# Kernel tuning notes

Measured on AMD Instinct MI355X. Metric: run time of the kernel, lower is better.

## Reference

```python
import jax, jax.numpy as jnp
import numpy as np

D_MODEL = 1024
NUM_HEADS = 16
D_K = D_MODEL // NUM_HEADS


def setup_inputs() -> dict:
    key = jax.random.key(0)
    ks = jax.random.split(key, 12)
    B, S = 2, 2048
    s = 1.0 / np.sqrt(D_MODEL)
    inp = {
        "query": jax.random.normal(ks[0], (B, S, D_MODEL), jnp.float32),
        "key": jax.random.normal(ks[1], (B, S, D_MODEL), jnp.float32),
        "value": jax.random.normal(ks[2], (B, S, D_MODEL), jnp.float32),
        "Wq": jax.random.normal(ks[3], (D_MODEL, D_MODEL), jnp.float32) * s,
        "bq": jax.random.normal(ks[4], (D_MODEL,), jnp.float32) * s,
        "Wk": jax.random.normal(ks[5], (D_MODEL, D_MODEL), jnp.float32) * s,
        "bk": jax.random.normal(ks[6], (D_MODEL,), jnp.float32) * s,
        "Wv": jax.random.normal(ks[7], (D_MODEL, D_MODEL), jnp.float32) * s,
        "bv": jax.random.normal(ks[8], (D_MODEL,), jnp.float32) * s,
        "Wo": jax.random.normal(ks[9], (D_MODEL, D_MODEL), jnp.float32) * s,
        "bo": jax.random.normal(ks[10], (D_MODEL,), jnp.float32) * s,
    }
    return inp


def _split_heads(x):
    B, S, _ = x.shape
    return x.reshape(B, S, NUM_HEADS, D_K).transpose(0, 2, 1, 3)  # [B,H,S,Dk]


def reference(query, key, value, Wq, bq, Wk, bk, Wv, bv, Wo, bo):
    # Linear projections (torch Linear: x @ W.T + b)
    Q = _split_heads(query @ Wq.T + bq)
    K = _split_heads(key @ Wk.T + bk)
    V = _split_heads(value @ Wv.T + bv)
    scale = 1.0 / jnp.sqrt(jnp.asarray(D_K, Q.dtype))
    scores = jnp.einsum('bhqd,bhkd->bhqk', Q, K) * scale  # [B,H,S,S]
    attn = jax.nn.softmax(scores, axis=-1)
    # dropout is identity in eval mode
    x = jnp.einsum('bhqk,bhkd->bhqd', attn, V)
    B, H, S, Dk = x.shape
    x = x.transpose(0, 2, 1, 3).reshape(B, S, H * Dk)
    return x @ Wo.T + bo
```

## Files before the change

kernel.cpp:

```cpp
#include <hip/hip_runtime.h>
#include <hip/hip_bf16.h>

typedef __bf16 bf16;
typedef __attribute__((ext_vector_type(4))) __bf16 bf16x4;
typedef __attribute__((ext_vector_type(8))) __bf16 bf16x8;
typedef __attribute__((ext_vector_type(4))) float f32x4;
typedef __attribute__((ext_vector_type(16))) float f32x16;
typedef unsigned int u32;

#define D_MODEL 1024
#define NHEADS 16
#define DK 64
#define BATCH 2
#define SEQ 2048
#define NTOK (BATCH * SEQ)

#define QSCALE 0.18033688011112042f
#define DEFER_THR 8.0f

__device__ __forceinline__ u32 cvtpk_bf16(float lo, float hi) {
  u32 r;
  asm("v_cvt_pk_bf16_f32 %0, %1, %2" : "=v"(r) : "v"(lo), "v"(hi));
  return r;
}
__device__ __forceinline__ void plswap(u32& a, u32& b) {
  asm("v_permlane32_swap_b32 %0, %1" : "+v"(a), "+v"(b));
}
__device__ __forceinline__ float fast_exp2(float x) {
#if __has_builtin(__builtin_amdgcn_exp2f)
  return __builtin_amdgcn_exp2f(x);
#else
  return exp2f(x);
#endif
}
__device__ __forceinline__ float xhalf_max(float x) {
  return fmaxf(x, __shfl_xor(x, 32));
}
__device__ __forceinline__ float xhalf_add(float x) {
  return x + __shfl_xor(x, 32);
}

__device__ __forceinline__ int frag_off_q(int s, int d) {
  return ((s >> 5) << 11) + ((d >> 4) << 9) + ((((d >> 3) & 1) * 32 + (s & 31)) << 3) + (d & 7);
}
__device__ __forceinline__ int frag_off_k(int s, int d) {
  return ((s >> 6) << 12) + ((((s >> 5) & 1) * 4 + (d >> 4)) << 9) +
         ((((d >> 3) & 1) * 32 + (s & 31)) << 3) + (d & 7);
}
__device__ __forceinline__ int frag_off_v(int s, int d) {
  return ((s >> 6) << 12) + (((d >> 5) * 4 + ((s >> 4) & 3)) << 9) +
         ((((s >> 3) & 1) * 32 + (d & 31)) << 3) + (s & 7);
}

__global__ __launch_bounds__(256) void cvt3_kernel(
    const float* __restrict__ s0, const float* __restrict__ s1, const float* __restrict__ s2,
    bf16* __restrict__ d0, bf16* __restrict__ d1, bf16* __restrict__ d2, int n4) {
  int i = blockIdx.x * blockDim.x + threadIdx.x;
  if (i >= n4) return;
  const float* s = blockIdx.y == 0 ? s0 : blockIdx.y == 1 ? s1 : s2;
  bf16* d = blockIdx.y == 0 ? d0 : blockIdx.y == 1 ? d1 : d2;
  float4 v = reinterpret_cast<const float4*>(s)[i];
  bf16x4 o;
  o[0] = (bf16)v.x; o[1] = (bf16)v.y; o[2] = (bf16)v.z; o[3] = (bf16)v.w;
  reinterpret_cast<bf16x4*>(d)[i] = o;
}

__global__ __launch_bounds__(256) void cvt4_kernel(
    const float* __restrict__ s0, const float* __restrict__ s1,
    const float* __restrict__ s2, const float* __restrict__ s3,
    bf16* __restrict__ d0, bf16* __restrict__ d1, bf16* __restrict__ d2, bf16* __restrict__ d3,
    int n4) {
  int i = blockIdx.x * blockDim.x + threadIdx.x;
  if (i >= n4) return;
  const float* s = blockIdx.y == 0 ? s0 : blockIdx.y == 1 ? s1 : blockIdx.y == 2 ? s2 : s3;
  bf16* d = blockIdx.y == 0 ? d0 : blockIdx.y == 1 ? d1 : blockIdx.y == 2 ? d2 : d3;
  float4 v = reinterpret_cast<const float4*>(s)[i];
  bf16x4 o;
  o[0] = (bf16)v.x; o[1] = (bf16)v.y; o[2] = (bf16)v.z; o[3] = (bf16)v.w;
  reinterpret_cast<bf16x4*>(d)[i] = o;
}

#define ASYNC_COPY16(gptr, lptr)                                                \
  __builtin_amdgcn_global_load_lds(                                             \
      (__attribute__((address_space(1))) void*)(gptr),                          \
      (__attribute__((address_space(3))) void*)(lptr), 16, 0, 0)

struct ProjArgs {
  const bf16* A[3];
  const bf16* W[3];
  const float* bias[3];
  bf16* out[3];
};

__global__ __launch_bounds__(256) void gemm_proj(ProjArgs pa, int K) {
  __shared__ bf16 As[128][32];
  __shared__ bf16 Bs[128][32];
  const int z = blockIdx.z;
  const bf16* A = pa.A[z];
  const bf16* Bw = pa.W[z];
  const int m0 = blockIdx.x * 128;
  const int n0 = blockIdx.y * 128;

  const int t = threadIdx.x;
  const int wave = t >> 6;
  const int lane = t & 63;
  const int wr = (wave >> 1) * 64;
  const int wc = (wave & 1) * 64;
  const int r4 = lane >> 2;
  const int c8 = (lane & 3) * 8;
  const int fr = lane & 15;
  const int fk = (lane >> 4) * 8;

  f32x4 acc[4][4] = {};

  for (int k0 = 0; k0 < K; k0 += 32) {
    ASYNC_COPY16(&A[(size_t)(m0 + wave * 16 + r4) * K + k0 + c8], &As[wave * 16][0]);
    ASYNC_COPY16(&A[(size_t)(m0 + 64 + wave * 16 + r4) * K + k0 + c8], &As[64 + wave * 16][0]);
    ASYNC_COPY16(&Bw[(size_t)(n0 + wave * 16 + r4) * K + k0 + c8], &Bs[wave * 16][0]);
    ASYNC_COPY16(&Bw[(size_t)(n0 + 64 + wave * 16 + r4) * K + k0 + c8], &Bs[64 + wave * 16][0]);
    __syncthreads();

    bf16x8 af[4], bfr[4];
#pragma unroll
    for (int m = 0; m < 4; m++)
      af[m] = *reinterpret_cast<const bf16x8*>(&As[wr + m * 16 + fr][fk]);
#pragma unroll
    for (int n = 0; n < 4; n++)
      bfr[n] = *reinterpret_cast<const bf16x8*>(&Bs[wc + n * 16 + fr][fk]);
#pragma unroll
    for (int m = 0; m < 4; m++)
#pragma unroll
      for (int n = 0; n < 4; n++)
        acc[m][n] = __builtin_amdgcn_mfma_f32_16x16x32_bf16(af[m], bfr[n], acc[m][n], 0, 0, 0);
    __syncthreads();
  }

  const float scale = (z == 0) ? QSCALE : 1.0f;
  const float* bias = pa.bias[z];
  bf16* out = pa.out[z];
#pragma unroll
  for (int m = 0; m < 4; m++) {
#pragma unroll
    for (int n = 0; n < 4; n++) {
      const int col = n0 + wc + n * 16 + fr;
      const float bv = bias[col];
#pragma unroll
      for (int j = 0; j < 4; j++) {
        const int row = m0 + wr + m * 16 + (lane >> 4) * 4 + j;
        const float v = (acc[m][n][j] + bv) * scale;
        const int b = row >> 11;
        const int s = row & (SEQ - 1);
        const int h = col >> 6;
        const int d = col & (DK - 1);
        const size_t base = (size_t)(b * NHEADS + h) * SEQ * DK;
        int off;
        if (z == 0)      off = frag_off_q(s, d);
        else if (z == 1) off = frag_off_k(s, d);
        else             off = frag_off_v(s, d);
        out[base + off] = (bf16)v;
      }
    }
  }
}

#define TM 128
#define TN 64
#define BK 32

__global__ __launch_bounds__(256) void gemm_out(
    const bf16* __restrict__ A, const bf16* __restrict__ Bw,
    const float* __restrict__ bias, float* __restrict__ out, int K) {
  __shared__ bf16 As[TM][BK];
  __shared__ bf16 Bs[TN][BK];
  const int m0 = blockIdx.x * TM;
  const int n0 = blockIdx.y * TN;

  const int t = threadIdx.x;
  const int wave = t >> 6;
  const int lane = t & 63;
  const int wr = (wave >> 1) * 64;
  const int wc = (wave & 1) * 32;
  const int r4 = lane >> 2;
  const int c8 = (lane & 3) * 8;
  const int fr = lane & 15;
  const int fk = (lane >> 4) * 8;

  f32x4 acc[4][2] = {};
  for (int k0 = 0; k0 < K; k0 += BK) {
    ASYNC_COPY16(&A[(size_t)(m0 + wave * 16 + r4) * K + k0 + c8], &As[wave * 16][0]);
    ASYNC_COPY16(&A[(size_t)(m0 + 64 + wave * 16 + r4) * K + k0 + c8], &As[64 + wave * 16][0]);
    ASYNC_COPY16(&Bw[(size_t)(n0 + wave * 16 + r4) * K + k0 + c8], &Bs[wave * 16][0]);
    __syncthreads();

    bf16x8 af[4], bfr[2];
#pragma unroll
    for (int m = 0; m < 4; m++)
      af[m] = *reinterpret_cast<const bf16x8*>(&As[wr + m * 16 + fr][fk]);
#pragma unroll
    for (int n = 0; n < 2; n++)
      bfr[n] = *reinterpret_cast<const bf16x8*>(&Bs[wc + n * 16 + fr][fk]);
#pragma unroll
    for (int m = 0; m < 4; m++)
#pragma unroll
      for (int n = 0; n < 2; n++)
        acc[m][n] = __builtin_amdgcn_mfma_f32_16x16x32_bf16(af[m], bfr[n], acc[m][n], 0, 0, 0);
    __syncthreads();
  }

#pragma unroll
  for (int m = 0; m < 4; m++) {
#pragma unroll
    for (int n = 0; n < 2; n++) {
      const int col = n0 + wc + n * 16 + fr;
      const float bv = bias[col];
#pragma unroll
      for (int j = 0; j < 4; j++) {
        const int row = m0 + wr + m * 16 + (lane >> 4) * 4 + j;
        out[(size_t)row * D_MODEL + col] = acc[m][n][j] + bv;
      }
    }
  }
}

#define QBLK 32
#define KVBLK 64
#define NT (SEQ / KVBLK)

__global__ __launch_bounds__(256, 2) void attn_kernel(
    const bf16* __restrict__ Qf,
    const bf16* __restrict__ Kf,
    const bf16* __restrict__ Vf,
    bf16* __restrict__ X) {
  const int lane = threadIdx.x & 63;
  const int wave = threadIdx.x >> 6;

  const int i = blockIdx.x;
  const int xcd = i & 7;
  const int slot = i >> 3;
  const int hgrp = slot >> 4;
  const int xq = slot & 15;
  const int bh = xcd + 8 * hgrp;
  const int bb = bh >> 4, hh = bh & (NHEADS - 1);
  const int q0 = xq * (QBLK * 4) + wave * QBLK;
  const int row = lane & 31, hi = lane >> 5;

  const bf16* Qp = Qf + (size_t)bh * SEQ * DK + (size_t)q0 * DK;
  const bf16* Kp = Kf + (size_t)bh * SEQ * DK;
  const bf16* Vp = Vf + (size_t)bh * SEQ * DK;

  bf16x8 qf[4];
#pragma unroll
  for (int kd = 0; kd < 4; kd++)
    qf[kd] = *reinterpret_cast<const bf16x8*>(&Qp[kd * 512 + lane * 8]);

  f32x16 ot0, ot1;
#pragma unroll
  for (int r = 0; r < 16; r++) { ot0[r] = 0.f; ot1[r] = 0.f; }
  float m_run = -1e30f, l_run = 0.f;

  bf16x8 ka[2][4], kb2[2][4];

#define LOADK(dst, tt)                                                          \
  {                                                                             \
    const bf16* kbase_ = Kp + (size_t)(tt) * 4096 + lane * 8;                   \
    _Pragma("unroll") for (int hf = 0; hf < 2; hf++)                            \
        _Pragma("unroll") for (int kd = 0; kd < 4; kd++)                        \
            dst[hf][kd] = *reinterpret_cast<const bf16x8*>(                     \
                &kbase_[(hf * 4 + kd) * 512]);                                  \
  }

  LOADK(ka, 0)
  LOADK(kb2, 1)
  f32x16 sa0, sa1, sb0, sb1;
#pragma unroll
  for (int r = 0; r < 16; r++) { sa0[r] = 0.f; sa1[r] = 0.f; }
  __builtin_amdgcn_s_setprio(1);
#pragma unroll
  for (int kd = 0; kd < 4; kd++)
    sa0 = __builtin_amdgcn_mfma_f32_32x32x16_bf16(ka[0][kd], qf[kd], sa0, 0, 0, 0);
#pragma unroll
  for (int kd = 0; kd < 4; kd++)
    sa1 = __builtin_amdgcn_mfma_f32_32x32x16_bf16(ka[1][kd], qf[kd], sa1, 0, 0, 0);
  __builtin_amdgcn_s_setprio(0);

  auto pipe = [&](f32x16& SC0, f32x16& SC1, f32x16& SN0, f32x16& SN1,
                  bf16x8 (&KN)[2][4], bf16x8 (&KL)[2][4], int tc) {
#pragma unroll
    for (int r = 0; r < 16; r++) { SN0[r] = 0.f; SN1[r] = 0.f; }
    __builtin_amdgcn_s_setprio(1);
#pragma unroll
    for (int kd = 0; kd < 4; kd++)
      SN0 = __builtin_amdgcn_mfma_f32_32x32x16_bf16(KN[0][kd], qf[kd], SN0, 0, 0, 0);
#pragma unroll
    for (int kd = 0; kd < 4; kd++)
      SN1 = __builtin_amdgcn_mfma_f32_32x32x16_bf16(KN[1][kd], qf[kd], SN1, 0, 0, 0);
    __builtin_amdgcn_s_setprio(0);

    LOADK(KL, (tc + 2) & (NT - 1))

    bf16x8 vf[2][4];
    {
      const bf16* vbase_ = Vp + (size_t)tc * 4096 + lane * 8;
#pragma unroll
      for (int dh = 0; dh < 2; dh++)
#pragma unroll
        for (int ks = 0; ks < 4; ks++)
          vf[dh][ks] = *reinterpret_cast<const bf16x8*>(&vbase_[(dh * 4 + ks) * 512]);
    }

    float w16[16];
#pragma unroll
    for (int r = 0; r < 16; r++) w16[r] = fmaxf(SC0[r], SC1[r]);
#pragma unroll
    for (int r = 0; r < 8; r++) w16[r] = fmaxf(w16[r], w16[r + 8]);
#pragma unroll
    for (int r = 0; r < 4; r++) w16[r] = fmaxf(w16[r], w16[r + 4]);
    float mx = fmaxf(fmaxf(w16[0], w16[1]), fmaxf(w16[2], w16[3]));
    mx = xhalf_max(mx);
    if (__any(mx > m_run + DEFER_THR)) {
      const float mn = fmaxf(m_run, mx);
      const float alpha = fast_exp2(m_run - mn);
      m_run = mn;
      l_run *= alpha;
#pragma unroll
      for (int r = 0; r < 16; r++) { ot0[r] *= alpha; ot1[r] *= alpha; }
    }
    float p[32];
#pragma unroll
    for (int r = 0; r < 16; r++) p[r] = fast_exp2(SC0[r] - m_run);
#pragma unroll
    for (int r = 0; r < 16; r++) p[16 + r] = fast_exp2(SC1[r] - m_run);
    float a16[16];
#pragma unroll
    for (int r = 0; r < 16; r++) a16[r] = p[r] + p[r + 16];
#pragma unroll
    for (int r = 0; r < 8; r++) a16[r] += a16[r + 8];
#pragma unroll
    for (int r = 0; r < 4; r++) a16[r] += a16[r + 4];
    float rs = (a16[0] + a16[1]) + (a16[2] + a16[3]);
    l_run += xhalf_add(rs);

    u32 c[16];
#pragma unroll
    for (int i2 = 0; i2 < 8; i2++) c[i2] = cvtpk_bf16(p[2 * i2], p[2 * i2 + 1]);
#pragma unroll
    for (int i2 = 0; i2 < 8; i2++) c[8 + i2] = cvtpk_bf16(p[16 + 2 * i2], p[17 + 2 * i2]);
    plswap(c[0], c[2]);   plswap(c[1], c[3]);
    plswap(c[4], c[6]);   plswap(c[5], c[7]);
    plswap(c[8], c[10]);  plswap(c[9], c[11]);
    plswap(c[12], c[14]); plswap(c[13], c[15]);
    bf16x8 pbv[4];
#pragma unroll
    for (int ks = 0; ks < 4; ks++) {
      union { u32 u[4]; bf16x8 v; } pk;
      pk.u[0] = c[ks * 4 + 0]; pk.u[1] = c[ks * 4 + 1];
      pk.u[2] = c[ks * 4 + 2]; pk.u[3] = c[ks * 4 + 3];
      pbv[ks] = pk.v;
    }

    __builtin_amdgcn_s_setprio(1);
#pragma unroll
    for (int ks = 0; ks < 4; ks++) {
      ot0 = __builtin_amdgcn_mfma_f32_32x32x16_bf16(vf[0][ks], pbv[ks], ot0, 0, 0, 0);
      ot1 = __builtin_amdgcn_mfma_f32_32x32x16_bf16(vf[1][ks], pbv[ks], ot1, 0, 0, 0);
    }
    __builtin_amdgcn_s_setprio(0);
  };

  for (int t = 0; t < NT; t += 2) {
    pipe(sa0, sa1, sb0, sb1, kb2, ka, t);
    pipe(sb0, sb1, sa0, sa1, ka, kb2, t + 1);
  }

  const float inv = 1.0f / l_run;
  bf16* Xp = X + ((size_t)bb * SEQ + q0 + row) * D_MODEL + hh * DK;
#pragma unroll
  for (int g = 0; g < 4; g++) {
    bf16x4 w0, w1;
#pragma unroll
    for (int j = 0; j < 4; j++) {
      w0[j] = (bf16)(ot0[g * 4 + j] * inv);
      w1[j] = (bf16)(ot1[g * 4 + j] * inv);
    }
    *reinterpret_cast<bf16x4*>(&Xp[g * 8 + hi * 4]) = w0;
    *reinterpret_cast<bf16x4*>(&Xp[32 + g * 8 + hi * 4]) = w1;
  }
}

extern "C" void kernel_launch(void* const* d_in, const int* in_sizes, int n_in,
                              void* d_out, int out_size, void* d_ws, size_t ws_size,
                              hipStream_t stream) {
  const float* q  = (const float*)d_in[0];
  const float* k  = (const float*)d_in[1];
  const float* v  = (const float*)d_in[2];
  const float* Wq = (const float*)d_in[3];
  const float* bq = (const float*)d_in[4];
  const float* Wk = (const float*)d_in[5];
  const float* bk = (const float*)d_in[6];
  const float* Wv = (const float*)d_in[7];
  const float* bv = (const float*)d_in[8];
  const float* Wo = (const float*)d_in[9];
  const float* bo = (const float*)d_in[10];

  char* ws = (char*)d_ws;
  size_t off = 0;
  auto alloc = [&](size_t bytes) -> void* {
    void* p = ws + off;
    off += (bytes + 255) & ~(size_t)255;
    return p;
  };
  const size_t ACT = (size_t)NTOK * D_MODEL;
  const size_t WEL = (size_t)D_MODEL * D_MODEL;

  bf16* Xq  = (bf16*)alloc(ACT * 2);
  bf16* Xk  = (bf16*)alloc(ACT * 2);
  bf16* Xv  = (bf16*)alloc(ACT * 2);
  bf16* Wqb = (bf16*)alloc(WEL * 2);
  bf16* Wkb = (bf16*)alloc(WEL * 2);
  bf16* Wvb = (bf16*)alloc(WEL * 2);
  bf16* Wob = (bf16*)alloc(WEL * 2);
  bf16* Qfb = (bf16*)alloc(ACT * 2);
  bf16* Kfb = (bf16*)alloc(ACT * 2);
  bf16* Vfb = (bf16*)alloc(ACT * 2);
  bf16* Xa  = (bf16*)alloc(ACT * 2);

  {
    int n4 = (int)(ACT / 4);
    cvt3_kernel<<<dim3((n4 + 255) / 256, 3), dim3(256), 0, stream>>>(q, k, v, Xq, Xk, Xv, n4);
  }
  {
    int n4 = (int)(WEL / 4);
    cvt4_kernel<<<dim3((n4 + 255) / 256, 4), dim3(256), 0, stream>>>(
        Wq, Wk, Wv, Wo, Wqb, Wkb, Wvb, Wob, n4);
  }

  ProjArgs pa;
  pa.A[0] = Xq;  pa.A[1] = Xk;  pa.A[2] = Xv;
  pa.W[0] = Wqb; pa.W[1] = Wkb; pa.W[2] = Wvb;
  pa.bias[0] = bq; pa.bias[1] = bk; pa.bias[2] = bv;
  pa.out[0] = Qfb; pa.out[1] = Kfb; pa.out[2] = Vfb;
  gemm_proj<<<dim3(NTOK / 128, D_MODEL / 128, 3), dim3(256), 0, stream>>>(pa, D_MODEL);

  attn_kernel<<<dim3(512), dim3(256), 0, stream>>>(Qfb, Kfb, Vfb, Xa);

  gemm_out<<<dim3(NTOK / TM, D_MODEL / TN), dim3(256), 0, stream>>>(
      Xa, Wob, bo, (float*)d_out, D_MODEL);
}
```

Baseline: 136.9 us.

## Halve attention KV tile to 32 and widen output GEMM tile to 128x128

The attention kernel now processes 32 keys per pipeline step instead of 64. This halves the score registers and K prefetch buffers, which lowers register pressure, but doubles the number of loop iterations and the online-softmax max checks. The output projection GEMM moves from 128x64 to 128x128 tiles with a 4x4 MFMA accumulator per wave. That gives more reuse per LDS load, but launches half as many blocks.

```diff
diff --git a/kernel.cpp b/kernel.cpp
--- a/kernel.cpp
+++ b/kernel.cpp
@@ -163,46 +163,44 @@
   }
 }
 
-#define TM 128
-#define TN 64
-#define BK 32
-
 __global__ __launch_bounds__(256) void gemm_out(
     const bf16* __restrict__ A, const bf16* __restrict__ Bw,
     const float* __restrict__ bias, float* __restrict__ out, int K) {
-  __shared__ bf16 As[TM][BK];
-  __shared__ bf16 Bs[TN][BK];
-  const int m0 = blockIdx.x * TM;
-  const int n0 = blockIdx.y * TN;
+  __shared__ bf16 As[128][32];
+  __shared__ bf16 Bs[128][32];
+  const int m0 = blockIdx.x * 128;
+  const int n0 = blockIdx.y * 128;
 
   const int t = threadIdx.x;
   const int wave = t >> 6;
   const int lane = t & 63;
   const int wr = (wave >> 1) * 64;
-  const int wc = (wave & 1) * 32;
+  const int wc = (wave & 1) * 64;
   const int r4 = lane >> 2;
   const int c8 = (lane & 3) * 8;
   const int fr = lane & 15;
   const int fk = (lane >> 4) * 8;
 
-  f32x4 acc[4][2] = {};
-  for (int k0 = 0; k0 < K; k0 += BK) {
+  f32x4 acc[4][4] = {};
+
+  for (int k0 = 0; k0 < K; k0 += 32) {
     ASYNC_COPY16(&A[(size_t)(m0 + wave * 16 + r4) * K + k0 + c8], &As[wave * 16][0]);
     ASYNC_COPY16(&A[(size_t)(m0 + 64 + wave * 16 + r4) * K + k0 + c8], &As[64 + wave * 16][0]);
     ASYNC_COPY16(&Bw[(size_t)(n0 + wave * 16 + r4) * K + k0 + c8], &Bs[wave * 16][0]);
+    ASYNC_COPY16(&Bw[(size_t)(n0 + 64 + wave * 16 + r4) * K + k0 + c8], &Bs[64 + wave * 16][0]);
     __syncthreads();
 
-    bf16x8 af[4], bfr[2];
+    bf16x8 af[4], bfr[4];
 #pragma unroll
     for (int m = 0; m < 4; m++)
       af[m] = *reinterpret_cast<const bf16x8*>(&As[wr + m * 16 + fr][fk]);
 #pragma unroll
-    for (int n = 0; n < 2; n++)
+    for (int n = 0; n < 4; n++)
       bfr[n] = *reinterpret_cast<const bf16x8*>(&Bs[wc + n * 16 + fr][fk]);
 #pragma unroll
     for (int m = 0; m < 4; m++)
 #pragma unroll
-      for (int n = 0; n < 2; n++)
+      for (int n = 0; n < 4; n++)
         acc[m][n] = __builtin_amdgcn_mfma_f32_16x16x32_bf16(af[m], bfr[n], acc[m][n], 0, 0, 0);
     __syncthreads();
   }
@@ -210,7 +208,7 @@
 #pragma unroll
   for (int m = 0; m < 4; m++) {
 #pragma unroll
-    for (int n = 0; n < 2; n++) {
+    for (int n = 0; n < 4; n++) {
       const int col = n0 + wc + n * 16 + fr;
       const float bv = bias[col];
 #pragma unroll
@@ -223,7 +221,7 @@
 }
 
 #define QBLK 32
-#define KVBLK 64
+#define KVBLK 32
 #define NT (SEQ / KVBLK)
 
 __global__ __launch_bounds__(256, 2) void attn_kernel(
@@ -258,64 +256,55 @@
   for (int r = 0; r < 16; r++) { ot0[r] = 0.f; ot1[r] = 0.f; }
   float m_run = -1e30f, l_run = 0.f;
 
-  bf16x8 ka[2][4], kb2[2][4];
-
-#define LOADK(dst, tt)                                                          \
+  bf16x8 ka[4], kb[4];
+
+#define LOADK32(dst, tt)                                                        \
   {                                                                             \
-    const bf16* kbase_ = Kp + (size_t)(tt) * 4096 + lane * 8;                   \
-    _Pragma("unroll") for (int hf = 0; hf < 2; hf++)                            \
-        _Pragma("unroll") for (int kd = 0; kd < 4; kd++)                        \
-            dst[hf][kd] = *reinterpret_cast<const bf16x8*>(                     \
-                &kbase_[(hf * 4 + kd) * 512]);                                  \
-  }
-
-  LOADK(ka, 0)
-  LOADK(kb2, 1)
-  f32x16 sa0, sa1, sb0, sb1;
-#pragma unroll
-  for (int r = 0; r < 16; r++) { sa0[r] = 0.f; sa1[r] = 0.f; }
+    const bf16* kbase_ = Kp + (size_t)(tt) * 2048 + lane * 8;                   \
+    _Pragma("unroll") for (int kd = 0; kd < 4; kd++)                            \
+        dst[kd] = *reinterpret_cast<const bf16x8*>(&kbase_[kd * 512]);          \
+  }
+
+  LOADK32(ka, 0)
+  LOADK32(kb, 1)
+  f32x16 sa, sb;
+#pragma unroll
+  for (int r = 0; r < 16; r++) sa[r] = 0.f;
   __builtin_amdgcn_s_setprio(1);
 #pragma unroll
   for (int kd = 0; kd < 4; kd++)
-    sa0 = __builtin_amdgcn_mfma_f32_32x32x16_bf16(ka[0][kd], qf[kd], sa0, 0, 0, 0);
-#pragma unroll
-  for (int kd = 0; kd < 4; kd++)
-    sa1 = __builtin_amdgcn_mfma_f32_32x32x16_bf16(ka[1][kd], qf[kd], sa1, 0, 0, 0);
+    sa = __builtin_amdgcn_mfma_f32_32x32x16_bf16(ka[kd], qf[kd], sa, 0, 0, 0);
   __builtin_amdgcn_s_setprio(0);
 
-  auto pipe = [&](f32x16& SC0, f32x16& SC1, f32x16& SN0, f32x16& SN1,
-                  bf16x8 (&KN)[2][4], bf16x8 (&KL)[2][4], int tc) {
-#pragma unroll
-    for (int r = 0; r < 16; r++) { SN0[r] = 0.f; SN1[r] = 0.f; }
+  auto pipe = [&](f32x16& SC, f32x16& SN, bf16x8 (&KN)[4], bf16x8 (&KL)[4], int tc) {
+#pragma unroll
+    for (int r = 0; r < 16; r++) SN[r] = 0.f;
     __builtin_amdgcn_s_setprio(1);
 #pragma unroll
     for (int kd = 0; kd < 4; kd++)
-      SN0 = __builtin_amdgcn_mfma_f32_32x32x16_bf16(KN[0][kd], qf[kd], SN0, 0, 0, 0);
-#pragma unroll
-    for (int kd = 0; kd < 4; kd++)
-      SN1 = __builtin_amdgcn_mfma_f32_32x32x16_bf16(KN[1][kd], qf[kd], SN1, 0, 0, 0);
+      SN = __builtin_amdgcn_mfma_f32_32x32x16_bf16(KN[kd], qf[kd], SN, 0, 0, 0);
     __builtin_amdgcn_s_setprio(0);
 
-    LOADK(KL, (tc + 2) & (NT - 1))
-
-    bf16x8 vf[2][4];
+    LOADK32(KL, (tc + 2) & (NT - 1))
+
+    bf16x8 vf[2][2];
     {
-      const bf16* vbase_ = Vp + (size_t)tc * 4096 + lane * 8;
+      const bf16* vbase_ = Vp + (size_t)(tc >> 1) * 4096 + lane * 8;
+      const int so = (tc & 1) * 2;
 #pragma unroll
       for (int dh = 0; dh < 2; dh++)
 #pragma unroll
-        for (int ks = 0; ks < 4; ks++)
-          vf[dh][ks] = *reinterpret_cast<const bf16x8*>(&vbase_[(dh * 4 + ks) * 512]);
-    }
-
-    float w16[16];
-#pragma unroll
-    for (int r = 0; r < 16; r++) w16[r] = fmaxf(SC0[r], SC1[r]);
-#pragma unroll
-    for (int r = 0; r < 8; r++) w16[r] = fmaxf(w16[r], w16[r + 8]);
-#pragma unroll
-    for (int r = 0; r < 4; r++) w16[r] = fmaxf(w16[r], w16[r + 4]);
-    float mx = fmaxf(fmaxf(w16[0], w16[1]), fmaxf(w16[2], w16[3]));
+        for (int ks = 0; ks < 2; ks++)
+          vf[dh][ks] = *reinterpret_cast<const bf16x8*>(
+              &vbase_[(dh * 4 + so + ks) * 512]);
+    }
+
+    float w8[8];
+#pragma unroll
+    for (int r = 0; r < 8; r++) w8[r] = fmaxf(SC[r], SC[r + 8]);
+#pragma unroll
+    for (int r = 0; r < 4; r++) w8[r] = fmaxf(w8[r], w8[r + 4]);
+    float mx = fmaxf(fmaxf(w8[0], w8[1]), fmaxf(w8[2], w8[3]));
     mx = xhalf_max(mx);
     if (__any(mx > m_run + DEFER_THR)) {
       const float mn = fmaxf(m_run, mx);
@@ -325,33 +314,25 @@
 #pragma unroll
       for (int r = 0; r < 16; r++) { ot0[r] *= alpha; ot1[r] *= alpha; }
     }
-    float p[32];
-#pragma unroll
-    for (int r = 0; r < 16; r++) p[r] = fast_exp2(SC0[r] - m_run);
-#pragma unroll
-    for (int r = 0; r < 16; r++) p[16 + r] = fast_exp2(SC1[r] - m_run);
-    float a16[16];
-#pragma unroll
-    for (int r = 0; r < 16; r++) a16[r] = p[r] + p[r + 16];
-#pragma unroll
-    for (int r = 0; r < 8; r++) a16[r] += a16[r + 8];
-#pragma unroll
-    for (int r = 0; r < 4; r++) a16[r] += a16[r + 4];
-    float rs = (a16[0] + a16[1]) + (a16[2] + a16[3]);
+    float p[16];
+#pragma unroll
+    for (int r = 0; r < 16; r++) p[r] = fast_exp2(SC[r] - m_run);
+    float a8[8];
+#pragma unroll
+    for (int r = 0; r < 8; r++) a8[r] = p[r] + p[r + 8];
+#pragma unroll
+    for (int r = 0; r < 4; r++) a8[r] += a8[r + 4];
+    float rs = (a8[0] + a8[1]) + (a8[2] + a8[3]);
     l_run += xhalf_add(rs);
 
-    u32 c[16];
+    u32 c[8];
 #pragma unroll
     for (int i2 = 0; i2 < 8; i2++) c[i2] = cvtpk_bf16(p[2 * i2], p[2 * i2 + 1]);
-#pragma unroll
-    for (int i2 = 0; i2 < 8; i2++) c[8 + i2] = cvtpk_bf16(p[16 + 2 * i2], p[17 + 2 * i2]);
     plswap(c[0], c[2]);   plswap(c[1], c[3]);
     plswap(c[4], c[6]);   plswap(c[5], c[7]);
-    plswap(c[8], c[10]);  plswap(c[9], c[11]);
-    plswap(c[12], c[14]); plswap(c[13], c[15]);
-    bf16x8 pbv[4];
-#pragma unroll
-    for (int ks = 0; ks < 4; ks++) {
+    bf16x8 pbv[2];
+#pragma unroll
+    for (int ks = 0; ks < 2; ks++) {
       union { u32 u[4]; bf16x8 v; } pk;
       pk.u[0] = c[ks * 4 + 0]; pk.u[1] = c[ks * 4 + 1];
       pk.u[2] = c[ks * 4 + 2]; pk.u[3] = c[ks * 4 + 3];
@@ -359,17 +340,16 @@
     }
 
     __builtin_amdgcn_s_setprio(1);
-#pragma unroll
-    for (int ks = 0; ks < 4; ks++) {
-      ot0 = __builtin_amdgcn_mfma_f32_32x32x16_bf16(vf[0][ks], pbv[ks], ot0, 0, 0, 0);
-      ot1 = __builtin_amdgcn_mfma_f32_32x32x16_bf16(vf[1][ks], pbv[ks], ot1, 0, 0, 0);
-    }
+    ot0 = __builtin_amdgcn_mfma_f32_32x32x16_bf16(vf[0][0], pbv[0], ot0, 0, 0, 0);
+    ot0 = __builtin_amdgcn_mfma_f32_32x32x16_bf16(vf[0][1], pbv[1], ot0, 0, 0, 0);
+    ot1 = __builtin_amdgcn_mfma_f32_32x32x16_bf16(vf[1][0], pbv[0], ot1, 0, 0, 0);
+    ot1 = __builtin_amdgcn_mfma_f32_32x32x16_bf16(vf[1][1], pbv[1], ot1, 0, 0, 0);
     __builtin_amdgcn_s_setprio(0);
   };
 
   for (int t = 0; t < NT; t += 2) {
-    pipe(sa0, sa1, sb0, sb1, kb2, ka, t);
-    pipe(sb0, sb1, sa0, sa1, ka, kb2, t + 1);
+    pipe(sa, sb, kb, ka, t);
+    pipe(sb, sa, ka, kb, t + 1);
   }
 
   const float inv = 1.0f / l_run;
@@ -443,6 +423,6 @@
 
   attn_kernel<<<dim3(512), dim3(256), 0, stream>>>(Qfb, Kfb, Vfb, Xa);
 
-  gemm_out<<<dim3(NTOK / TM, D_MODEL / TN), dim3(256), 0, stream>>>(
+  gemm_out<<<dim3(NTOK / 128, D_MODEL / 128), dim3(256), 0, stream>>>(
       Xa, Wob, bo, (float*)d_out, D_MODEL);
 }
```

Measured after the change: 138.2 us. About the same (+1.0%).
